# Kernel tuning notes

Measured on AMD Instinct MI355X. Metric: run time of the kernel, lower is better.

## Reference

```python
import jax, jax.numpy as jnp
import numpy as np

NUM_NODES = 200000
NUM_EDGES = 300000
NUM_QUERIES = 128
NUM_ENTITIES = 50000
N_DIMS = 256
N_DIMS_SM = 64
STATIC_DIM = 128
STATIC_SM = 32
G_IN = 2 * N_DIMS_SM + STATIC_SM + N_DIMS_SM  # 224


def leaky(x):
    return jnp.where(x > 0, x, 0.01 * x)


def setup_inputs() -> dict:
    key = jax.random.key(0)
    ks = jax.random.split(key, 24)
    W = 0.05  # weight scale to keep logits in a sane range
    inp = {
        'memorized_embedding': jax.random.normal(ks[0], (NUM_NODES, N_DIMS), jnp.float32),
        'node_score': jax.random.uniform(ks[1], (NUM_NODES,), jnp.float32),
        'rel_emb': jax.random.normal(ks[2], (NUM_EDGES, N_DIMS), jnp.float32),
        'query_src_ts_emb': jax.random.normal(ks[3], (NUM_QUERIES, STATIC_DIM), jnp.float32),
        'query_rel_emb': jax.random.normal(ks[4], (NUM_QUERIES, N_DIMS), jnp.float32),
        'eg_idx': jax.random.randint(ks[5], (NUM_EDGES,), 0, NUM_QUERIES, jnp.int32),
        'src_idx': jax.random.randint(ks[6], (NUM_EDGES,), 0, NUM_NODES, jnp.int32),
        'dst_idx': jax.random.randint(ks[7], (NUM_EDGES,), 0, NUM_NODES, jnp.int32),
        'entity_idx': jax.random.randint(ks[8], (NUM_NODES,), 0, NUM_ENTITIES, jnp.int32),
        'W_proj': W * jax.random.normal(ks[9], (N_DIMS, N_DIMS_SM), jnp.float32),
        'b_proj': W * jax.random.normal(ks[10], (N_DIMS_SM,), jnp.float32),
        'W_static': W * jax.random.normal(ks[11], (STATIC_DIM, STATIC_SM), jnp.float32),
        'b_static': W * jax.random.normal(ks[12], (STATIC_SM,), jnp.float32),
        'W_bs': W * jax.random.normal(ks[13], (N_DIMS, N_DIMS), jnp.float32),
        'b_bs': W * jax.random.normal(ks[14], (N_DIMS,), jnp.float32),
        'Wl': W * jax.random.normal(ks[15], (G_IN, N_DIMS_SM), jnp.float32),
        'bl': W * jax.random.normal(ks[16], (N_DIMS_SM,), jnp.float32),
        'Wr': W * jax.random.normal(ks[17], (G_IN, N_DIMS_SM), jnp.float32),
        'br': W * jax.random.normal(ks[18], (N_DIMS_SM,), jnp.float32),
        'Wc': W * jax.random.normal(ks[19], (N_DIMS_SM, N_DIMS_SM), jnp.float32),
        'bc': W * jax.random.normal(ks[20], (N_DIMS_SM,), jnp.float32),
    }
    return inp


def reference(memorized_embedding, node_score, rel_emb, query_src_ts_emb, query_rel_emb,
              eg_idx, src_idx, dst_idx, entity_idx,
              W_proj, b_proj, W_static, b_static, W_bs, b_bs,
              Wl, bl, Wr, br, Wc, bc):
    # one attention-flow step: linear_between_steps -> attention scoring (G) ->
    # per-source-node softmax -> attention propagation -> per-entity aggregation
    emb2 = leaky(memorized_embedding @ W_bs + b_bs)        # [N, d]
    # project all node embeddings once (linear commutes with gather)
    proj_all = emb2 @ W_proj + b_proj                       # [N, d_sm]
    hvi = proj_all[src_idx]                                 # [E, d_sm]
    hvj = proj_all[dst_idx]                                 # [E, d_sm]
    rel = rel_emb @ W_proj + b_proj                         # [E, d_sm]
    # context_dim_red
    qs = query_src_ts_emb @ W_static + b_static             # [B, static_sm]
    qr = query_rel_emb @ W_proj + b_proj                    # [B, d_sm]
    qs_e = qs[eg_idx]                                       # [E, static_sm]
    qr_e = qr[eg_idx]                                       # [E, d_sm]
    left = jnp.concatenate([hvi, rel, qs_e, qr_e], axis=-1)   # [E, G_IN]
    right = jnp.concatenate([hvj, rel, qs_e, qr_e], axis=-1)  # [E, G_IN]
    # G: sum(leaky(left W_l) * ((leaky(right W_r)) W_c))
    lh = leaky(left @ Wl + bl)                              # [E, d_sm]
    rh = leaky(right @ Wr + br) @ Wc + bc                   # [E, d_sm]
    logits = jnp.sum(lh * rh, axis=-1)                      # [E]
    # transition probability: softmax over outgoing edges of each source node
    seg_max = jax.ops.segment_max(logits, src_idx, num_segments=NUM_NODES)
    ex = jnp.exp(logits - seg_max[src_idx])
    denom = jax.ops.segment_sum(ex, src_idx, num_segments=NUM_NODES)
    trans = ex / denom[src_idx]
    # propagate node attention along edges (node_score_aggregation='sum')
    new_node_score = jax.ops.segment_sum(trans * node_score[src_idx], dst_idx,
                                         num_segments=NUM_NODES)
    # _aggregate_op_entity: sparse COO matmul == segment_sum over entity groups
    entity_att_score = jax.ops.segment_sum(new_node_score, entity_idx,
                                           num_segments=NUM_ENTITIES)
    return entity_att_score
```

## Files before the change

### kernel.cpp

```cpp
#include <hip/hip_runtime.h>
#include <hip/hip_bf16.h>

#define N_NODES 200000
#define N_EDGES 300000
#define N_Q     128
#define N_ENT   50000
#define D       256
#define DSM     64
#define SDIM    128
#define SSM     32

#define NODE_BLKS 6250
#define REL_BLKS  9375
#define GROUPS    3125

typedef __attribute__((ext_vector_type(8))) short bf16x8;
typedef __attribute__((ext_vector_type(4))) float f32x4;

__device__ __forceinline__ float leaky(float x){ return x > 0.f ? x : 0.01f*x; }

__device__ __forceinline__ unsigned short f2bf(float f){
  __hip_bfloat16 h = __float2bfloat16(f);
  return *reinterpret_cast<unsigned short*>(&h);
}
__device__ __forceinline__ unsigned pk2bf(float a, float b){
  float2 t; t.x = a; t.y = b;
  __hip_bfloat162 h = __float22bfloat162_rn(t);
  return *reinterpret_cast<unsigned*>(&h);
}
__device__ __forceinline__ float bf2f(unsigned short h){
  return __uint_as_float(((unsigned)h) << 16);
}

__device__ __forceinline__ void dev_pack(const float* __restrict__ src,
                                         unsigned short* __restrict__ dst,
                                         int K, int N, int id, int total){
  if (id >= total) return;
  int lane = id & 63, fb = id >> 6;
  int KB = K >> 5;
  int kb = fb % KB, nb = fb / KB;
  int k0 = kb*32 + ((lane>>4)<<3);
  int n  = nb*16 + (lane & 15);
  #pragma unroll
  for (int i = 0; i < 8; ++i) dst[(size_t)id*8 + i] = f2bf(src[(size_t)(k0+i)*N + n]);
}

__global__ void k_setup1(float* out, float* denom,
                         const float* __restrict__ Wp, const float* __restrict__ Wl,
                         const float* __restrict__ Wr, float* Wnlr, float* Wrlr,
                         const float* __restrict__ bp, float* cv,
                         const float* __restrict__ qsrc, const float* __restrict__ Ws,
                         const float* __restrict__ bs, const float* __restrict__ qrel,
                         float* qs, float* qr,
                         const float* __restrict__ Wbs, unsigned short* Wbs_pk,
                         const float* __restrict__ Wc, unsigned short* Wc_pk){
  int b = blockIdx.x, tid = threadIdx.x;
  if (b < 782){
    int id = b*256 + tid;
    if (id < N_ENT) out[id] = 0.f;
    if (id < N_NODES) denom[id] = 0.f;
  } else if (b < 1038){
    int id = (b-782)*256 + tid;
    int m = id >> 14, rem = id & 16383, k = rem >> 6, c = rem & 63;
    const float* Wsrc = (m & 1) ? Wr : Wl;
    int roff = (m >> 1) * 64;
    float s = 0.f;
    for (int i = 0; i < 64; ++i) s += Wp[k*64+i] * Wsrc[(roff+i)*64 + c];
    float* o = (m >> 1) ? Wrlr : Wnlr;
    o[k*128 + (m&1)*64 + c] = s;
  } else if (b == 1038){
    int m = tid >> 6, c = tid & 63;
    const float* Wsrc = (m & 1) ? Wr : Wl;
    int roff = (m >> 1) * 64;
    float s = 0.f;
    for (int i = 0; i < 64; ++i) s += bp[i] * Wsrc[(roff+i)*64 + c];
    cv[tid] = s;
  } else if (b < 1087){
    int id = (b-1039)*256 + tid;
    if (id < N_Q*SSM){
      int q = id >> 5, i = id & 31;
      float s = bs[i];
      for (int j = 0; j < SDIM; ++j) s += qsrc[q*SDIM+j] * Ws[j*SSM+i];
      qs[id] = s;
    } else {
      int id2 = id - N_Q*SSM;
      int q = id2 >> 6, i = id2 & 63;
      float s = bp[i];
      for (int j = 0; j < D; ++j) s += qrel[q*D+j] * Wp[j*DSM+i];
      qr[id2] = s;
    }
  } else if (b < 1119){
    dev_pack(Wbs, Wbs_pk, 256, 256, (b-1087)*256 + tid, 8192);
  } else {
    dev_pack(Wc, Wc_pk, 64, 64, (b-1119)*256 + tid, 512);
  }
}

__global__ void k_setup2(const float* __restrict__ qs, const float* __restrict__ qr,
                         const float* __restrict__ Wl, const float* __restrict__ bl,
                         const float* __restrict__ Wr, const float* __restrict__ br,
                         unsigned* qctx_p,
                         const float* __restrict__ Wnlr, unsigned short* Wn_pk,
                         const float* __restrict__ Wrlr, unsigned short* Wr_pk){
  int b = blockIdx.x, tid = threadIdx.x;
  if (b < 32){
    int id = b*256 + tid;
    int q = id >> 6, c = id & 63;
    float sl = bl[c], sr = br[c];
    for (int i = 0; i < SSM; ++i){
      float v = qs[q*SSM+i];
      sl += v * Wl[(128+i)*64+c];
      sr += v * Wr[(128+i)*64+c];
    }
    for (int i = 0; i < DSM; ++i){
      float v = qr[q*DSM+i];
      sl += v * Wl[(160+i)*64+c];
      sr += v * Wr[(160+i)*64+c];
    }
    qctx_p[id] = pk2bf(sl, sr);
  } else if (b < 48){
    dev_pack(Wnlr, Wn_pk, 256, 128, (b-32)*256 + tid, 4096);
  } else {
    dev_pack(Wrlr, Wr_pk, 256, 128, (b-48)*256 + tid, 4096);
  }
}

__global__ __launch_bounds__(256) void k_proj(const float* __restrict__ A,
    const unsigned short* __restrict__ Wbs_pk, const float* __restrict__ bbs,
    const unsigned short* __restrict__ Wn_pk, const float* __restrict__ cv,
    unsigned short* __restrict__ node_l, unsigned short* __restrict__ node_r,
    const float* __restrict__ relE, const unsigned short* __restrict__ Wr_pk,
    unsigned* __restrict__ rel_pk){
  __shared__ char smem[16384];
  int tid = threadIdx.x;
  int l = tid & 63, wn = tid >> 6;
  int g = blockIdx.x / 5, r5 = blockIdx.x % 5;

  if (r5 < 2){
    int row0 = (g*2 + r5) * 32;
    {
      const float4* Ag = (const float4*)(A + (size_t)row0 * 256);
      #pragma unroll
      for (int it = 0; it < 8; ++it){
        int f = tid + 256*it;
        int r = f >> 6, c4 = f & 63;
        float4 v = Ag[f];
        uint2 u;
        u.x = pk2bf(v.x, v.y);
        u.y = pk2bf(v.z, v.w);
        int byte = (r << 9) + (c4 << 3);
        byte ^= (r & 7) << 4;
        *(uint2*)(smem + byte) = u;
      }
    }
    __syncthreads();
    f32x4 acc[2][4];
    #pragma unroll
    for (int mf = 0; mf < 2; ++mf)
      #pragma unroll
      for (int nf = 0; nf < 4; ++nf) acc[mf][nf] = (f32x4){0.f,0.f,0.f,0.f};
    for (int kb = 0; kb < 8; ++kb){
      bf16x8 a[2], b[4];
      #pragma unroll
      for (int mf = 0; mf < 2; ++mf){
        int row = mf*16 + (l & 15);
        int byte = (row << 9) + kb*64 + ((l >> 4) << 4);
        byte ^= (row & 7) << 4;
        a[mf] = *(const bf16x8*)(smem + byte);
      }
      #pragma unroll
      for (int nf = 0; nf < 4; ++nf){
        int nbb = wn*4 + nf;
        b[nf] = *(const bf16x8*)(Wbs_pk + ((size_t)(nbb*8 + kb)*64 + l)*8);
      }
      #pragma unroll
      for (int mf = 0; mf < 2; ++mf)
        #pragma unroll
        for (int nf = 0; nf < 4; ++nf)
          acc[mf][nf] = __builtin_amdgcn_mfma_f32_16x16x32_bf16(a[mf], b[nf], acc[mf][nf], 0, 0, 0);
    }
    __syncthreads();
    #pragma unroll
    for (int mf = 0; mf < 2; ++mf)
      #pragma unroll
      for (int nf = 0; nf < 4; ++nf){
        int col = wn*64 + nf*16 + (l & 15);
        float bb = bbs[col];
        #pragma unroll
        for (int r = 0; r < 4; ++r){
          int row = mf*16 + ((l >> 4) << 2) + r;
          int byte = (row << 9) + col*2;
          byte ^= (row & 7) << 4;
          *(unsigned short*)(smem + byte) = f2bf(leaky(acc[mf][nf][r] + bb));
        }
      }
    __syncthreads();
    f32x4 acc2[2][2];
    #pragma unroll
    for (int mf = 0; mf < 2; ++mf){ acc2[mf][0] = (f32x4){0.f,0.f,0.f,0.f}; acc2[mf][1] = (f32x4){0.f,0.f,0.f,0.f}; }
    for (int kb = 0; kb < 8; ++kb){
      bf16x8 a[2], b[2];
      #pragma unroll
      for (int mf = 0; mf < 2; ++mf){
        int row = mf*16 + (l & 15);
        int byte = (row << 9) + kb*64 + ((l >> 4) << 4);
        byte ^= (row & 7) << 4;
        a[mf] = *(const bf16x8*)(smem + byte);
      }
      #pragma unroll
      for (int nf = 0; nf < 2; ++nf){
        int nbb = wn*2 + nf;
        b[nf] = *(const bf16x8*)(Wn_pk + ((size_t)(nbb*8 + kb)*64 + l)*8);
      }
      #pragma unroll
      for (int mf = 0; mf < 2; ++mf)
        #pragma unroll
        for (int nf = 0; nf < 2; ++nf)
          acc2[mf][nf] = __builtin_amdgcn_mfma_f32_16x16x32_bf16(a[mf], b[nf], acc2[mf][nf], 0, 0, 0);
    }
    #pragma unroll
    for (int mf = 0; mf < 2; ++mf)
      #pragma unroll
      for (int nf = 0; nf < 2; ++nf){
        int col = wn*32 + nf*16 + (l & 15);
        float cc = cv[col];
        #pragma unroll
        for (int r = 0; r < 4; ++r){
          int row = mf*16 + ((l >> 4) << 2) + r;
          unsigned short h = f2bf(acc2[mf][nf][r] + cc);
          size_t gg = (size_t)(row0 + row);
          if (col < 64) node_l[gg*64 + col] = h;
          else          node_r[gg*64 + col - 64] = h;
        }
      }
  } else {
    int row0 = (g*3 + (r5 - 2)) * 32;
    {
      const float4* Rg = (const float4*)(relE + (size_t)row0 * 256);
      #pragma unroll
      for (int it = 0; it < 8; ++it){
        int f = tid + 256*it;
        int r = f >> 6, c4 = f & 63;
        float4 v = Rg[f];
        uint2 u;
        u.x = pk2bf(v.x, v.y);
        u.y = pk2bf(v.z, v.w);
        int byte = (r << 9) + (c4 << 3);
        byte ^= (r & 7) << 4;
        *(uint2*)(smem + byte) = u;
      }
    }
    __syncthreads();
    f32x4 acc[2][2];
    #pragma unroll
    for (int mf = 0; mf < 2; ++mf){ acc[mf][0] = (f32x4){0.f,0.f,0.f,0.f}; acc[mf][1] = (f32x4){0.f,0.f,0.f,0.f}; }
    for (int kb = 0; kb < 8; ++kb){
      bf16x8 a[2], b0, b1;
      #pragma unroll
      for (int mf = 0; mf < 2; ++mf){
        int row = mf*16 + (l & 15);
        int byte = (row << 9) + kb*64 + ((l >> 4) << 4);
        byte ^= (row & 7) << 4;
        a[mf] = *(const bf16x8*)(smem + byte);
      }
      b0 = *(const bf16x8*)(Wr_pk + ((size_t)(wn*8 + kb)*64 + l)*8);
      b1 = *(const bf16x8*)(Wr_pk + ((size_t)((4+wn)*8 + kb)*64 + l)*8);
      #pragma unroll
      for (int mf = 0; mf < 2; ++mf){
        acc[mf][0] = __builtin_amdgcn_mfma_f32_16x16x32_bf16(a[mf], b0, acc[mf][0], 0, 0, 0);
        acc[mf][1] = __builtin_amdgcn_mfma_f32_16x16x32_bf16(a[mf], b1, acc[mf][1], 0, 0, 0);
      }
    }
    int c = wn*16 + (l & 15);
    float cvL = cv[128 + c], cvR = cv[192 + c];
    #pragma unroll
    for (int mf = 0; mf < 2; ++mf)
      #pragma unroll
      for (int r = 0; r < 4; ++r){
        int row = mf*16 + ((l >> 4) << 2) + r;
        rel_pk[(size_t)(row0 + row)*64 + c] = pk2bf(acc[mf][0][r] + cvL, acc[mf][1][r] + cvR);
      }
  }
}

__global__ __launch_bounds__(256, 4) void k_score(const unsigned* __restrict__ rel_pk,
    const unsigned short* __restrict__ Wc_pk, const float* __restrict__ bc,
    const unsigned short* __restrict__ node_l, const unsigned short* __restrict__ node_r,
    const unsigned* __restrict__ qctx_p,
    const int* __restrict__ src, const int* __restrict__ dst, const int* __restrict__ eg,
    float* __restrict__ exbuf, float* __restrict__ denom){
  __shared__ char smem[16384];
  int tid = threadIdx.x;
  int l = tid & 63, wn = tid >> 6;
  char* wbase = smem + wn*4096;
  char* sLc  = wbase;
  char* sRin = wbase + 2048;
  int e0 = blockIdx.x * 64 + wn*16;

  int idxv;
  {
    int j = l & 15;
    int e = e0 + j;
    int ec = e < N_EDGES ? e : N_EDGES-1;
    const int* p = (l < 16) ? src : (l < 32) ? dst : eg;
    idxv = p[ec];
  }
  unsigned rlrv[16];
  unsigned short nlv[16], nrv[16];
  #pragma unroll
  for (int j = 0; j < 16; ++j){
    int e = e0 + j;
    int ec = e < N_EDGES ? e : N_EDGES-1;
    rlrv[j] = rel_pk[(size_t)ec*64 + l];
    int s  = __shfl(idxv, j);
    int d2 = __shfl(idxv, 16 + j);
    nlv[j] = node_l[(size_t)s*64 + l];
    nrv[j] = node_r[(size_t)d2*64 + l];
  }
  #pragma unroll
  for (int j = 0; j < 16; ++j){
    int e = e0 + j;
    int bL = (j << 7) + (l << 1);  bL ^= (j & 12) << 3;
    int bR = (j << 7) + (l << 1);  bR ^= (j & 7) << 4;
    unsigned short lh16 = 0, rr16 = 0;
    if (e < N_EDGES){
      int b = __shfl(idxv, 32 + j);
      unsigned qv = qctx_p[b*64 + l];
      unsigned rv = rlrv[j];
      float lh = leaky(bf2f(nlv[j]) + bf2f((unsigned short)(rv & 0xFFFFu))
                       + bf2f((unsigned short)(qv & 0xFFFFu)));
      float rr = leaky(bf2f(nrv[j]) + bf2f((unsigned short)(rv >> 16))
                       + bf2f((unsigned short)(qv >> 16)));
      lh16 = f2bf(lh); rr16 = f2bf(rr);
    }
    *(unsigned short*)(sLc + bL) = lh16;
    *(unsigned short*)(sRin + bR) = rr16;
  }
  float bcv[4];
  #pragma unroll
  for (int nf = 0; nf < 4; ++nf) bcv[nf] = bc[nf*16 + (l & 15)];
  f32x4 acc2[4];
  #pragma unroll
  for (int nf = 0; nf < 4; ++nf) acc2[nf] = (f32x4){0.f,0.f,0.f,0.f};
  #pragma unroll
  for (int kb = 0; kb < 2; ++kb){
    int row = l & 15;
    int byte = (row << 7) + kb*64 + ((l >> 4) << 4);
    byte ^= (row & 7) << 4;
    bf16x8 a = *(const bf16x8*)(sRin + byte);
    #pragma unroll
    for (int nf = 0; nf < 4; ++nf){
      bf16x8 bfr = *(const bf16x8*)(Wc_pk + ((size_t)(nf*2 + kb)*64 + l)*8);
      acc2[nf] = __builtin_amdgcn_mfma_f32_16x16x32_bf16(a, bfr, acc2[nf], 0, 0, 0);
    }
  }
  int srcj[4];
  float vr[4];
  #pragma unroll
  for (int r = 0; r < 4; ++r){
    int rowl = ((l >> 4) << 2) + r;
    srcj[r] = __shfl(idxv, rowl);
    float v = 0.f;
    #pragma unroll
    for (int nf = 0; nf < 4; ++nf){
      int col = nf*16 + (l & 15);
      int byte = (rowl << 7) + (col << 1);
      byte ^= (rowl & 12) << 3;
      v += (acc2[nf][r] + bcv[nf]) * bf2f(*(unsigned short*)(sLc + byte));
    }
    v += __shfl_xor(v, 1); v += __shfl_xor(v, 2);
    v += __shfl_xor(v, 4); v += __shfl_xor(v, 8);
    vr[r] = v;
  }
  if ((l & 15) == 0){
    #pragma unroll
    for (int r = 0; r < 4; ++r){
      int rowl = ((l >> 4) << 2) + r;
      int e = e0 + rowl;
      if (e < N_EDGES){
        float ex = __expf(vr[r]);
        exbuf[e] = ex;
        atomicAdd(&denom[srcj[r]], ex);
      }
    }
  }
}

__global__ void k_passC(const float* __restrict__ exbuf, const float* __restrict__ denom,
                        const int* __restrict__ src, const int* __restrict__ dst,
                        const float* __restrict__ node_score, const int* __restrict__ ent,
                        float* __restrict__ out){
  int e = blockIdx.x*256 + threadIdx.x;
  if (e >= N_EDGES) return;
  int s = src[e];
  float tr = exbuf[e] / denom[s];
  atomicAdd(&out[ent[dst[e]]], tr * node_score[s]);
}

extern "C" void kernel_launch(void* const* d_in, const int* in_sizes, int n_in,
                              void* d_out, int out_size, void* d_ws, size_t ws_size,
                              hipStream_t stream){
  const float* mem   = (const float*)d_in[0];
  const float* nsc   = (const float*)d_in[1];
  const float* relE  = (const float*)d_in[2];
  const float* qsrc  = (const float*)d_in[3];
  const float* qrel  = (const float*)d_in[4];
  const int*   eg    = (const int*)d_in[5];
  const int*   src   = (const int*)d_in[6];
  const int*   dst   = (const int*)d_in[7];
  const int*   ent   = (const int*)d_in[8];
  const float* Wp    = (const float*)d_in[9];
  const float* bp    = (const float*)d_in[10];
  const float* Ws    = (const float*)d_in[11];
  const float* bs    = (const float*)d_in[12];
  const float* Wbs   = (const float*)d_in[13];
  const float* bbs   = (const float*)d_in[14];
  const float* Wl    = (const float*)d_in[15];
  const float* bl    = (const float*)d_in[16];
  const float* Wr    = (const float*)d_in[17];
  const float* br    = (const float*)d_in[18];
  const float* Wc    = (const float*)d_in[19];
  const float* bc    = (const float*)d_in[20];
  float* out = (float*)d_out;

  char* w = (char*)d_ws;
  auto alloc = [&](size_t bytes)->void*{
    void* p = (void*)w; w += (bytes + 255) & ~(size_t)255; return p;
  };
  float* Wnlr = (float*)alloc(32768*4);
  float* Wrlr = (float*)alloc(32768*4);
  unsigned short* Wbs_pk = (unsigned short*)alloc(65536*2);
  unsigned short* Wn_pk  = (unsigned short*)alloc(32768*2);
  unsigned short* Wr_pk  = (unsigned short*)alloc(32768*2);
  unsigned short* Wc_pk  = (unsigned short*)alloc(4096*2);
  float* cv  = (float*)alloc(256*4);
  float* qs  = (float*)alloc((size_t)N_Q*SSM*4);
  float* qr  = (float*)alloc((size_t)N_Q*DSM*4);
  unsigned* qctx_p = (unsigned*)alloc((size_t)N_Q*DSM*4);
  unsigned short* node_l = (unsigned short*)alloc((size_t)N_NODES*64*2);
  unsigned short* node_r = (unsigned short*)alloc((size_t)N_NODES*64*2);
  unsigned* rel_pk = (unsigned*)alloc((size_t)N_EDGES*64*4);
  float* exbuf  = (float*)alloc((size_t)N_EDGES*4);
  float* denom = (float*)alloc((size_t)N_NODES*4);

  k_setup1<<<1121, 256, 0, stream>>>(out, denom,
                                     Wp, Wl, Wr, Wnlr, Wrlr, bp, cv,
                                     qsrc, Ws, bs, qrel, qs, qr,
                                     Wbs, Wbs_pk, Wc, Wc_pk);
  k_setup2<<<64, 256, 0, stream>>>(qs, qr, Wl, bl, Wr, br, qctx_p,
                                   Wnlr, Wn_pk, Wrlr, Wr_pk);
  k_proj<<<GROUPS*5, 256, 0, stream>>>(mem, Wbs_pk, bbs, Wn_pk, cv, node_l, node_r,
                                       relE, Wr_pk, rel_pk);
  k_score<<<(N_EDGES+63)/64, 256, 0, stream>>>(rel_pk, Wc_pk, bc, node_l, node_r, qctx_p,
                                               src, dst, eg, exbuf, denom);
  k_passC<<<(N_EDGES+255)/256, 256, 0, stream>>>(exbuf, denom, src, dst, nsc, ent, out);
}
```

Measured before the change: 236.4 us.

## Make projection kernel persistent with double-buffered LDS tile prefetch

Replaces the one-tile-per-block projection grid with a persistent grid of 1024 groups that loop over node and relation tiles. The next tile's fp32 rows are loaded into registers while the current tile's MFMA work runs from one of two LDS buffers. This is meant to hide global load latency and cut per-block launch and ramp overhead. In exchange it doubles LDS per block to 32KB, raises register pressure, and leaves some blocks with uneven tile counts.

```diff
diff --git a/kernel.cpp b/kernel.cpp
--- a/kernel.cpp
+++ b/kernel.cpp
@@ -10,12 +10,17 @@
 #define SDIM    128
 #define SSM     32
 
-#define NODE_BLKS 6250
-#define REL_BLKS  9375
-#define GROUPS    3125
+#define NODE_TILES 6250
+#define REL_TILES  9375
+#define NW_NODE    2048
+#define NW_REL     3072
+#define GRID_GROUPS 1024
 
 typedef __attribute__((ext_vector_type(8))) short bf16x8;
 typedef __attribute__((ext_vector_type(4))) float f32x4;
+
+#define LGKM_BAR() do{ asm volatile("s_waitcnt lgkmcnt(0)" ::: "memory"); \
+  __builtin_amdgcn_s_barrier(); __builtin_amdgcn_sched_barrier(0); }while(0)
 
 __device__ __forceinline__ float leaky(float x){ return x > 0.f ? x : 0.01f*x; }
 
@@ -131,155 +136,179 @@
     unsigned short* __restrict__ node_l, unsigned short* __restrict__ node_r,
     const float* __restrict__ relE, const unsigned short* __restrict__ Wr_pk,
     unsigned* __restrict__ rel_pk){
-  __shared__ char smem[16384];
+  __shared__ char smem[32768];
   int tid = threadIdx.x;
   int l = tid & 63, wn = tid >> 6;
   int g = blockIdx.x / 5, r5 = blockIdx.x % 5;
 
+  auto stage_write = [&](float4* v, char* nbuf){
+    #pragma unroll
+    for (int it = 0; it < 8; ++it){
+      int f = tid + 256*it;
+      int r = f >> 6, c4 = f & 63;
+      uint2 u; u.x = pk2bf(v[it].x, v[it].y); u.y = pk2bf(v[it].z, v[it].w);
+      int byte = (r << 9) + (c4 << 3);
+      byte ^= (r & 7) << 4;
+      *(uint2*)(nbuf + byte) = u;
+    }
+  };
+
   if (r5 < 2){
-    int row0 = (g*2 + r5) * 32;
-    {
-      const float4* Ag = (const float4*)(A + (size_t)row0 * 256);
-      #pragma unroll
-      for (int it = 0; it < 8; ++it){
-        int f = tid + 256*it;
-        int r = f >> 6, c4 = f & 63;
-        float4 v = Ag[f];
-        uint2 u;
-        u.x = pk2bf(v.x, v.y);
-        u.y = pk2bf(v.z, v.w);
-        int byte = (r << 9) + (c4 << 3);
-        byte ^= (r & 7) << 4;
-        *(uint2*)(smem + byte) = u;
+    int w = g*2 + r5;
+    const float4* Abase = (const float4*)A;
+
+    auto nodeCompute = [&](int row0, char* buf){
+      f32x4 acc[2][4];
+      #pragma unroll
+      for (int mf = 0; mf < 2; ++mf)
+        #pragma unroll
+        for (int nf = 0; nf < 4; ++nf) acc[mf][nf] = (f32x4){0.f,0.f,0.f,0.f};
+      for (int kb = 0; kb < 8; ++kb){
+        bf16x8 a[2], b[4];
+        #pragma unroll
+        for (int mf = 0; mf < 2; ++mf){
+          int row = mf*16 + (l & 15);
+          int byte = (row << 9) + kb*64 + ((l >> 4) << 4);
+          byte ^= (row & 7) << 4;
+          a[mf] = *(const bf16x8*)(buf + byte);
+        }
+        #pragma unroll
+        for (int nf = 0; nf < 4; ++nf){
+          int nbb = wn*4 + nf;
+          b[nf] = *(const bf16x8*)(Wbs_pk + ((size_t)(nbb*8 + kb)*64 + l)*8);
+        }
+        #pragma unroll
+        for (int mf = 0; mf < 2; ++mf)
+          #pragma unroll
+          for (int nf = 0; nf < 4; ++nf)
+            acc[mf][nf] = __builtin_amdgcn_mfma_f32_16x16x32_bf16(a[mf], b[nf], acc[mf][nf], 0, 0, 0);
       }
-    }
-    __syncthreads();
-    f32x4 acc[2][4];
-    #pragma unroll
-    for (int mf = 0; mf < 2; ++mf)
-      #pragma unroll
-      for (int nf = 0; nf < 4; ++nf) acc[mf][nf] = (f32x4){0.f,0.f,0.f,0.f};
-    for (int kb = 0; kb < 8; ++kb){
-      bf16x8 a[2], b[4];
-      #pragma unroll
-      for (int mf = 0; mf < 2; ++mf){
-        int row = mf*16 + (l & 15);
-        int byte = (row << 9) + kb*64 + ((l >> 4) << 4);
-        byte ^= (row & 7) << 4;
-        a[mf] = *(const bf16x8*)(smem + byte);
+      LGKM_BAR();
+      #pragma unroll
+      for (int mf = 0; mf < 2; ++mf)
+        #pragma unroll
+        for (int nf = 0; nf < 4; ++nf){
+          int col = wn*64 + nf*16 + (l & 15);
+          float bb = bbs[col];
+          #pragma unroll
+          for (int r = 0; r < 4; ++r){
+            int row = mf*16 + ((l >> 4) << 2) + r;
+            int byte = (row << 9) + col*2;
+            byte ^= (row & 7) << 4;
+            *(unsigned short*)(buf + byte) = f2bf(leaky(acc[mf][nf][r] + bb));
+          }
+        }
+      LGKM_BAR();
+      f32x4 acc2[2][2];
+      #pragma unroll
+      for (int mf = 0; mf < 2; ++mf){ acc2[mf][0] = (f32x4){0.f,0.f,0.f,0.f}; acc2[mf][1] = (f32x4){0.f,0.f,0.f,0.f}; }
+      for (int kb = 0; kb < 8; ++kb){
+        bf16x8 a[2], b[2];
+        #pragma unroll
+        for (int mf = 0; mf < 2; ++mf){
+          int row = mf*16 + (l & 15);
+          int byte = (row << 9) + kb*64 + ((l >> 4) << 4);
+          byte ^= (row & 7) << 4;
+          a[mf] = *(const bf16x8*)(buf + byte);
+        }
+        #pragma unroll
+        for (int nf = 0; nf < 2; ++nf){
+          int nbb = wn*2 + nf;
+          b[nf] = *(const bf16x8*)(Wn_pk + ((size_t)(nbb*8 + kb)*64 + l)*8);
+        }
+        #pragma unroll
+        for (int mf = 0; mf < 2; ++mf)
+          #pragma unroll
+          for (int nf = 0; nf < 2; ++nf)
+            acc2[mf][nf] = __builtin_amdgcn_mfma_f32_16x16x32_bf16(a[mf], b[nf], acc2[mf][nf], 0, 0, 0);
       }
       #pragma unroll
-      for (int nf = 0; nf < 4; ++nf){
-        int nbb = wn*4 + nf;
-        b[nf] = *(const bf16x8*)(Wbs_pk + ((size_t)(nbb*8 + kb)*64 + l)*8);
+      for (int mf = 0; mf < 2; ++mf)
+        #pragma unroll
+        for (int nf = 0; nf < 2; ++nf){
+          int col = wn*32 + nf*16 + (l & 15);
+          float cc = cv[col];
+          #pragma unroll
+          for (int r = 0; r < 4; ++r){
+            int row = mf*16 + ((l >> 4) << 2) + r;
+            unsigned short h = f2bf(acc2[mf][nf][r] + cc);
+            size_t gg = (size_t)(row0 + row);
+            if (col < 64) node_l[gg*64 + col] = h;
+            else          node_r[gg*64 + col - 64] = h;
+          }
+        }
+    };
+
+    float4 v[8];
+    #pragma unroll
+    for (int it = 0; it < 8; ++it) v[it] = Abase[(size_t)w*2048 + tid + 256*it];
+    stage_write(v, smem);
+    int cur = 0;
+    int t = w;
+    for (; t + NW_NODE < NODE_TILES; t += NW_NODE){
+      #pragma unroll
+      for (int it = 0; it < 8; ++it)
+        v[it] = Abase[(size_t)(t + NW_NODE)*2048 + tid + 256*it];
+      LGKM_BAR();
+      nodeCompute(t*32, smem + (cur << 14));
+      stage_write(v, smem + ((cur ^ 1) << 14));
+      cur ^= 1;
+    }
+    LGKM_BAR();
+    nodeCompute(t*32, smem + (cur << 14));
+  } else {
+    int w = g*3 + (r5 - 2);
+    const float4* Rbase = (const float4*)relE;
+
+    auto relCompute = [&](int row0, char* buf){
+      f32x4 acc[2][2];
+      #pragma unroll
+      for (int mf = 0; mf < 2; ++mf){ acc[mf][0] = (f32x4){0.f,0.f,0.f,0.f}; acc[mf][1] = (f32x4){0.f,0.f,0.f,0.f}; }
+      for (int kb = 0; kb < 8; ++kb){
+        bf16x8 a[2], b0, b1;
+        #pragma unroll
+        for (int mf = 0; mf < 2; ++mf){
+          int row = mf*16 + (l & 15);
+          int byte = (row << 9) + kb*64 + ((l >> 4) << 4);
+          byte ^= (row & 7) << 4;
+          a[mf] = *(const bf16x8*)(buf + byte);
+        }
+        b0 = *(const bf16x8*)(Wr_pk + ((size_t)(wn*8 + kb)*64 + l)*8);
+        b1 = *(const bf16x8*)(Wr_pk + ((size_t)((4+wn)*8 + kb)*64 + l)*8);
+        #pragma unroll
+        for (int mf = 0; mf < 2; ++mf){
+          acc[mf][0] = __builtin_amdgcn_mfma_f32_16x16x32_bf16(a[mf], b0, acc[mf][0], 0, 0, 0);
+          acc[mf][1] = __builtin_amdgcn_mfma_f32_16x16x32_bf16(a[mf], b1, acc[mf][1], 0, 0, 0);
+        }
       }
+      int c = wn*16 + (l & 15);
+      float cvL = cv[128 + c], cvR = cv[192 + c];
       #pragma unroll
       for (int mf = 0; mf < 2; ++mf)
-        #pragma unroll
-        for (int nf = 0; nf < 4; ++nf)
-          acc[mf][nf] = __builtin_amdgcn_mfma_f32_16x16x32_bf16(a[mf], b[nf], acc[mf][nf], 0, 0, 0);
-    }
-    __syncthreads();
-    #pragma unroll
-    for (int mf = 0; mf < 2; ++mf)
-      #pragma unroll
-      for (int nf = 0; nf < 4; ++nf){
-        int col = wn*64 + nf*16 + (l & 15);
-        float bb = bbs[col];
         #pragma unroll
         for (int r = 0; r < 4; ++r){
           int row = mf*16 + ((l >> 4) << 2) + r;
-          int byte = (row << 9) + col*2;
-          byte ^= (row & 7) << 4;
-          *(unsigned short*)(smem + byte) = f2bf(leaky(acc[mf][nf][r] + bb));
-        }
-      }
-    __syncthreads();
-    f32x4 acc2[2][2];
-    #pragma unroll
-    for (int mf = 0; mf < 2; ++mf){ acc2[mf][0] = (f32x4){0.f,0.f,0.f,0.f}; acc2[mf][1] = (f32x4){0.f,0.f,0.f,0.f}; }
-    for (int kb = 0; kb < 8; ++kb){
-      bf16x8 a[2], b[2];
-      #pragma unroll
-      for (int mf = 0; mf < 2; ++mf){
-        int row = mf*16 + (l & 15);
-        int byte = (row << 9) + kb*64 + ((l >> 4) << 4);
-        byte ^= (row & 7) << 4;
-        a[mf] = *(const bf16x8*)(smem + byte);
-      }
-      #pragma unroll
-      for (int nf = 0; nf < 2; ++nf){
-        int nbb = wn*2 + nf;
-        b[nf] = *(const bf16x8*)(Wn_pk + ((size_t)(nbb*8 + kb)*64 + l)*8);
-      }
-      #pragma unroll
-      for (int mf = 0; mf < 2; ++mf)
-        #pragma unroll
-        for (int nf = 0; nf < 2; ++nf)
-          acc2[mf][nf] = __builtin_amdgcn_mfma_f32_16x16x32_bf16(a[mf], b[nf], acc2[mf][nf], 0, 0, 0);
-    }
-    #pragma unroll
-    for (int mf = 0; mf < 2; ++mf)
-      #pragma unroll
-      for (int nf = 0; nf < 2; ++nf){
-        int col = wn*32 + nf*16 + (l & 15);
-        float cc = cv[col];
-        #pragma unroll
-        for (int r = 0; r < 4; ++r){
-          int row = mf*16 + ((l >> 4) << 2) + r;
-          unsigned short h = f2bf(acc2[mf][nf][r] + cc);
-          size_t gg = (size_t)(row0 + row);
-          if (col < 64) node_l[gg*64 + col] = h;
-          else          node_r[gg*64 + col - 64] = h;
-        }
-      }
-  } else {
-    int row0 = (g*3 + (r5 - 2)) * 32;
-    {
-      const float4* Rg = (const float4*)(relE + (size_t)row0 * 256);
-      #pragma unroll
-      for (int it = 0; it < 8; ++it){
-        int f = tid + 256*it;
-        int r = f >> 6, c4 = f & 63;
-        float4 v = Rg[f];
-        uint2 u;
-        u.x = pk2bf(v.x, v.y);
-        u.y = pk2bf(v.z, v.w);
-        int byte = (r << 9) + (c4 << 3);
-        byte ^= (r & 7) << 4;
-        *(uint2*)(smem + byte) = u;
-      }
-    }
-    __syncthreads();
-    f32x4 acc[2][2];
-    #pragma unroll
-    for (int mf = 0; mf < 2; ++mf){ acc[mf][0] = (f32x4){0.f,0.f,0.f,0.f}; acc[mf][1] = (f32x4){0.f,0.f,0.f,0.f}; }
-    for (int kb = 0; kb < 8; ++kb){
-      bf16x8 a[2], b0, b1;
-      #pragma unroll
-      for (int mf = 0; mf < 2; ++mf){
-        int row = mf*16 + (l & 15);
-        int byte = (row << 9) + kb*64 + ((l >> 4) << 4);
-        byte ^= (row & 7) << 4;
-        a[mf] = *(const bf16x8*)(smem + byte);
-      }
-      b0 = *(const bf16x8*)(Wr_pk + ((size_t)(wn*8 + kb)*64 + l)*8);
-      b1 = *(const bf16x8*)(Wr_pk + ((size_t)((4+wn)*8 + kb)*64 + l)*8);
-      #pragma unroll
-      for (int mf = 0; mf < 2; ++mf){
-        acc[mf][0] = __builtin_amdgcn_mfma_f32_16x16x32_bf16(a[mf], b0, acc[mf][0], 0, 0, 0);
-        acc[mf][1] = __builtin_amdgcn_mfma_f32_16x16x32_bf16(a[mf], b1, acc[mf][1], 0, 0, 0);
-      }
-    }
-    int c = wn*16 + (l & 15);
-    float cvL = cv[128 + c], cvR = cv[192 + c];
-    #pragma unroll
-    for (int mf = 0; mf < 2; ++mf)
-      #pragma unroll
-      for (int r = 0; r < 4; ++r){
-        int row = mf*16 + ((l >> 4) << 2) + r;
-        rel_pk[(size_t)(row0 + row)*64 + c] = pk2bf(acc[mf][0][r] + cvL, acc[mf][1][r] + cvR);
-      }
+          rel_pk[(size_t)(row0 + row)*64 + c] = pk2bf(acc[mf][0][r] + cvL, acc[mf][1][r] + cvR);
+        }
+    };
+
+    float4 v[8];
+    #pragma unroll
+    for (int it = 0; it < 8; ++it) v[it] = Rbase[(size_t)w*2048 + tid + 256*it];
+    stage_write(v, smem);
+    int cur = 0;
+    int t = w;
+    for (; t + NW_REL < REL_TILES; t += NW_REL){
+      #pragma unroll
+      for (int it = 0; it < 8; ++it)
+        v[it] = Rbase[(size_t)(t + NW_REL)*2048 + tid + 256*it];
+      LGKM_BAR();
+      relCompute(t*32, smem + (cur << 14));
+      stage_write(v, smem + ((cur ^ 1) << 14));
+      cur ^= 1;
+    }
+    LGKM_BAR();
+    relCompute(t*32, smem + (cur << 14));
   }
 }
 
@@ -449,8 +478,8 @@
                                      Wbs, Wbs_pk, Wc, Wc_pk);
   k_setup2<<<64, 256, 0, stream>>>(qs, qr, Wl, bl, Wr, br, qctx_p,
                                    Wnlr, Wn_pk, Wrlr, Wr_pk);
-  k_proj<<<GROUPS*5, 256, 0, stream>>>(mem, Wbs_pk, bbs, Wn_pk, cv, node_l, node_r,
-                                       relE, Wr_pk, rel_pk);
+  k_proj<<<GRID_GROUPS*5, 256, 0, stream>>>(mem, Wbs_pk, bbs, Wn_pk, cv, node_l, node_r,
+                                            relE, Wr_pk, rel_pk);
   k_score<<<(N_EDGES+63)/64, 256, 0, stream>>>(rel_pk, Wc_pk, bc, node_l, node_r, qctx_p,
                                                src, dst, eg, exbuf, denom);
   k_passC<<<(N_EDGES+255)/256, 256, 0, stream>>>(exbuf, denom, src, dst, nsc, ent, out);
```

Measured after the change: 312.2 us. +32.1%, slower.
